# Optimization experiments

Hardware: AMD Instinct MI355X
Metric: run time of the kernel (lower is better)

The kernel has to match this reference:

```python
import jax, jax.numpy as jnp
import numpy as np

VOCAB = 50000
EMB = 200        # embedding_size
CAP = 3          # capitalization_size
IN = EMB + CAP   # LSTM input size = 203
HID = 128        # LSTMCell(128)
B = 256
T = 500          # comment_length
NC = 6           # num_classes
DENSE = 64


def _lstm_scan(x_tbi, W, b):
    """x_tbi: [T,B,IN]. W: [IN+HID, 4*HID] (tf gate order i, j, f, o), b: [4*HID].
    Returns h sequence [T,B,HID]. forget_bias=1.0 as in tf.contrib.rnn.LSTMCell."""
    h0 = jnp.zeros((x_tbi.shape[1], HID), x_tbi.dtype)

    def step(carry, x):
        h, c = carry
        gates = jnp.concatenate([x, h], axis=-1) @ W + b   # [B, 4*HID]
        i, j, f, o = jnp.split(gates, 4, axis=-1)
        c = jax.nn.sigmoid(f + 1.0) * c + jax.nn.sigmoid(i) * jnp.tanh(j)
        h = jax.nn.sigmoid(o) * jnp.tanh(c)
        return (h, c), h

    _, hs = jax.lax.scan(step, (h0, h0), x_tbi)
    return hs


def setup_inputs() -> dict:
    key = jax.random.key(0)
    ks = jax.random.split(key, 12)
    words = jax.random.randint(ks[0], (B, T), 0, VOCAB, dtype=jnp.int32)
    capitals = jax.random.randint(ks[1], (B, T), 0, CAP, dtype=jnp.int32)
    # word embeddings: random trainable table with a trailing zero-padding row
    word_emb = jax.random.normal(ks[2], (VOCAB + 1, EMB), dtype=jnp.float32) * 0.1
    # capitalization embedding: one_hot_embedding_matrix(3) = [eye(3); zeros(1,3)]
    cap_emb = jnp.concatenate([jnp.eye(CAP, dtype=jnp.float32),
                               jnp.zeros((1, CAP), dtype=jnp.float32)], axis=0)
    def glorot(k, shape):
        lim = np.sqrt(6.0 / (shape[0] + shape[1]))
        return jax.random.uniform(k, shape, jnp.float32, -lim, lim)
    W_fw = glorot(ks[3], (IN + HID, 4 * HID))
    b_fw = jnp.zeros((4 * HID,), jnp.float32)
    W_bw = glorot(ks[4], (IN + HID, 4 * HID))
    b_bw = jnp.zeros((4 * HID,), jnp.float32)
    W1 = glorot(ks[5], (2 * HID, DENSE))
    b1 = jnp.zeros((DENSE,), jnp.float32)
    W2 = glorot(ks[6], (DENSE, NC))
    b2 = jnp.zeros((NC,), jnp.float32)
    return {"words": words, "capitals": capitals, "word_emb": word_emb,
            "cap_emb": cap_emb, "W_fw": W_fw, "b_fw": b_fw,
            "W_bw": W_bw, "b_bw": b_bw, "W1": W1, "b1": b1,
            "W2": W2, "b2": b2}


def reference(words, capitals, word_emb, cap_emb, W_fw, b_fw, W_bw, b_bw,
              W1, b1, W2, b2):
    # embedding lookups and concat -> [B, T, 203]
    x = jnp.concatenate([word_emb[words], cap_emb[capitals]], axis=-1)
    x_tbi = jnp.transpose(x, (1, 0, 2))                    # [T, B, IN]
    # forward direction: take output at last timestep
    h_fw_last = _lstm_scan(x_tbi, W_fw, b_fw)[-1]          # [B, HID]
    # backward direction: bidirectional_dynamic_rnn reverses bw outputs back,
    # so outputs[1][:, 0, :] == last state of scan over the reversed sequence
    h_bw_first = _lstm_scan(x_tbi[::-1], W_bw, b_bw)[-1]   # [B, HID]
    rnn_output = jnp.concatenate([h_fw_last, h_bw_first], axis=1)  # [B, 256]
    dense1 = jax.nn.elu(rnn_output @ W1 + b1)              # [B, 64]
    y_hat = jax.nn.sigmoid(dense1 @ W2 + b2)               # [B, NC]
    return y_hat
```

## Files before the change

kernel.cpp:

```cpp
#include <hip/hip_runtime.h>

#define T 500
#define NB 256
#define VROWS 50001
#define EMB 200
#define KPAD 224
#define MPAD 50048

typedef unsigned short u16;
typedef __attribute__((ext_vector_type(8))) __bf16 bf16x8;
typedef __attribute__((ext_vector_type(8))) short short8;
typedef __attribute__((ext_vector_type(4))) float f32x4;
typedef __attribute__((ext_vector_type(4))) u16 u16x4;
typedef __attribute__((ext_vector_type(4))) int i32x4;

__device__ __forceinline__ u16 f2bf(float x) {
  __bf16 h = (__bf16)x;
  return __builtin_bit_cast(u16, h);
}
__device__ __forceinline__ float bf2f(u16 b) {
  union { unsigned u; float f; } v; v.u = ((unsigned)b) << 16;
  return v.f;
}
__device__ __forceinline__ float rcp_(float x) { return __builtin_amdgcn_rcpf(x); }
__device__ __forceinline__ float sig_(float x) { return rcp_(1.f + __expf(-x)); }
__device__ __forceinline__ float tanh_(float x) { return 1.f - 2.f * rcp_(1.f + __expf(2.f * x)); }

__global__ void prep_kernel(const int* __restrict__ words, const int* __restrict__ caps,
                            const float* __restrict__ word_emb,
                            const float* __restrict__ cap_emb,
                            const float* __restrict__ Wfw, const float* __restrict__ bfw,
                            const float* __restrict__ Wbw, const float* __restrict__ bbw,
                            int* __restrict__ wordsT, int* __restrict__ capsT,
                            float* __restrict__ Cproj, u16* __restrict__ Apad,
                            u16* __restrict__ Bt) {
  const int S0 = NB * T;
  const int S1 = MPAD * (KPAD / 4);
  const int S2 = 2 * 512 * KPAD;
  const int S3 = 2 * 4 * 512;
  int tid = blockIdx.x * blockDim.x + threadIdx.x;
  int nthr = gridDim.x * blockDim.x;
  for (int i = tid; i < S0 + S1 + S2 + S3; i += nthr) {
    if (i < S0) {
      int b = i / T, t = i - b * T;
      wordsT[t * NB + b] = words[i];
      capsT[t * NB + b]  = caps[i];
    } else if (i < S0 + S1) {
      int idx = i - S0;
      int v = idx / (KPAD / 4), q = idx - v * (KPAD / 4);
      int k = q * 4;
      u16x4 o;
      if (v < VROWS && k < EMB) {
        const float* p = word_emb + (size_t)v * EMB + k;
        o[0] = f2bf(p[0]); o[1] = f2bf(p[1]); o[2] = f2bf(p[2]); o[3] = f2bf(p[3]);
      } else {
        o[0] = o[1] = o[2] = o[3] = 0;
      }
      *(u16x4*)(Apad + (size_t)v * KPAD + k) = o;
    } else if (i < S0 + S1 + S2) {
      int idx = i - S0 - S1;
      int d = idx / (512 * KPAD), rem = idx - d * (512 * KPAD);
      int colp = rem / KPAD, k = rem - colp * KPAD;
      const float* W = d ? Wbw : Wfw;
      int g = colp & 3, jj = colp >> 2;
      Bt[idx] = (k < EMB) ? f2bf(W[k * 512 + g * 128 + jj]) : (u16)0;
    } else {
      int idx = i - S0 - S1 - S2;
      int dir = idx >> 11; int c = (idx >> 9) & 3; int colp = idx & 511;
      int j = colp >> 2, g = colp & 3;
      const float* W = dir ? Wbw : Wfw;
      const float* bias = dir ? bbw : bfw;
      float v = bias[g * 128 + j];
      #pragma unroll
      for (int cc = 0; cc < 3; ++cc)
        v += cap_emb[c * 3 + cc] * W[(200 + cc) * 512 + g * 128 + j];
      Cproj[idx] = v;
    }
  }
}

__global__ __launch_bounds__(256) void vproj_kernel(
    const u16* __restrict__ Apad, const u16* __restrict__ Bt,
    u16* __restrict__ Vfw, u16* __restrict__ Vbw) {
  const int mt = blockIdx.x, nt = blockIdx.y, dir = blockIdx.z;
  const u16* __restrict__ B = Bt + (size_t)dir * 512 * KPAD;
  u16* __restrict__ V = dir ? Vbw : Vfw;

  __shared__ u16 Al[2][128 * 32];
  __shared__ u16 Bl[2][128 * 32];

  const int tid = threadIdx.x;
  const int w = tid >> 6, l = tid & 63;
  const int la = l & 15, lb = l >> 4;
  const int m0 = mt * 128, n0 = nt * 128;

  auto stage = [&](int buf, int ks) {
    int k0 = ks * 32;
    #pragma unroll
    for (int h = 0; h < 2; ++h) {
      int c = w * 128 + h * 64 + l;
      int row = c >> 2, kq = c & 3;
      const u16* ga = Apad + (size_t)(m0 + row) * KPAD + k0 + kq * 8;
      __builtin_amdgcn_global_load_lds(
          (const __attribute__((address_space(1))) void*)ga,
          (__attribute__((address_space(3))) void*)&Al[buf][(w * 128 + h * 64) * 8],
          16, 0, 0);
      const u16* gb = B + (size_t)(n0 + row) * KPAD + k0 + kq * 8;
      __builtin_amdgcn_global_load_lds(
          (const __attribute__((address_space(1))) void*)gb,
          (__attribute__((address_space(3))) void*)&Bl[buf][(w * 128 + h * 64) * 8],
          16, 0, 0);
    }
  };

  f32x4 z = {0.f, 0.f, 0.f, 0.f};
  f32x4 acc[4][4] = {{z,z,z,z},{z,z,z,z},{z,z,z,z},{z,z,z,z}};
  const int wr = w >> 1, wc = w & 1;

  stage(0, 0);
  __syncthreads();
  #pragma unroll 1
  for (int ks = 0; ks < 7; ++ks) {
    int cur = ks & 1;
    if (ks < 6) stage(cur ^ 1, ks + 1);
    bf16x8 af[4], bfr[4];
    #pragma unroll
    for (int m = 0; m < 4; ++m)
      af[m] = *(const bf16x8*)&Al[cur][(wr * 64 + m * 16 + la) * 32 + lb * 8];
    #pragma unroll
    for (int n = 0; n < 4; ++n)
      bfr[n] = *(const bf16x8*)&Bl[cur][(wc * 64 + n * 16 + la) * 32 + lb * 8];
    #pragma unroll
    for (int m = 0; m < 4; ++m)
      #pragma unroll
      for (int n = 0; n < 4; ++n)
        acc[m][n] = __builtin_amdgcn_mfma_f32_16x16x32_bf16(af[m], bfr[n], acc[m][n], 0, 0, 0);
    __syncthreads();
  }

  #pragma unroll
  for (int m = 0; m < 4; ++m) {
    #pragma unroll
    for (int n = 0; n < 4; ++n) {
      #pragma unroll
      for (int r = 0; r < 4; ++r) {
        int v = m0 + wr * 64 + m * 16 + lb * 4 + r;
        int colp = n0 + wc * 64 + n * 16 + la;
        V[(size_t)v * 512 + colp] = f2bf(acc[m][n][r]);
      }
    }
  }
}

template <int PAR>
__device__ __forceinline__ void lstm_step(
    int t, int dir, int b0, int la, int lb, int j,
    const int* __restrict__ wordsT, const int* __restrict__ capsT,
    const u16* __restrict__ V, const float* __restrict__ Cp,
    const bf16x8 (&bfrag)[4][4], u16* __restrict__ hbuf,
    u16x4 (&vw_c)[4], f32x4 (&cp_c)[4],
    i32x4& wi_c, i32x4& ci_c,
    i32x4& wi_g, i32x4& ci_g,
    u16x4 (&vw_g)[4], f32x4 (&cp_g)[4],
    f32x4& cst, f32x4& hl) {
  {
    int ts = t + 4; if (ts > T - 1) ts = T - 1;
    int tt = dir ? (T - 1 - ts) : ts;
    wi_c = *(const i32x4*)(wordsT + tt * NB + b0 + lb * 4);
    ci_c = *(const i32x4*)(capsT + tt * NB + b0 + lb * 4);
  }
  #pragma unroll
  for (int r = 0; r < 4; ++r) {
    vw_g[r] = *(const u16x4*)(V + (size_t)wi_g[r] * 512 + j * 4);
    cp_g[r] = *(const f32x4*)(Cp + ci_g[r] * 512 + j * 4);
  }

  const u16* hb = hbuf + PAR * 2048;
  const int swz = (la & 7) << 3;
  bf16x8 afr[4];
  #pragma unroll
  for (int kk = 0; kk < 4; ++kk)
    afr[kk] = *(const bf16x8*)(hb + ((la * 128 + kk * 32 + lb * 8) ^ swz));

  f32x4 acc0, acc1, acc2, acc3;
  #pragma unroll
  for (int r = 0; r < 4; ++r) {
    acc0[r] = bf2f(vw_c[r][0]) + cp_c[r][0];
    acc1[r] = bf2f(vw_c[r][1]) + cp_c[r][1];
    acc2[r] = bf2f(vw_c[r][2]) + cp_c[r][2];
    acc3[r] = bf2f(vw_c[r][3]) + cp_c[r][3];
  }
  #pragma unroll
  for (int kk = 0; kk < 4; ++kk) {
    acc0 = __builtin_amdgcn_mfma_f32_16x16x32_bf16(afr[kk], bfrag[0][kk], acc0, 0, 0, 0);
    acc1 = __builtin_amdgcn_mfma_f32_16x16x32_bf16(afr[kk], bfrag[1][kk], acc1, 0, 0, 0);
    acc2 = __builtin_amdgcn_mfma_f32_16x16x32_bf16(afr[kk], bfrag[2][kk], acc2, 0, 0, 0);
    acc3 = __builtin_amdgcn_mfma_f32_16x16x32_bf16(afr[kk], bfrag[3][kk], acc3, 0, 0, 0);
  }
  u16* ho = hbuf + (PAR ^ 1) * 2048;
  #pragma unroll
  for (int r = 0; r < 4; ++r) {
    float fg = sig_(acc2[r] + 1.f);
    float ig = sig_(acc0[r]);
    float tj = tanh_(acc1[r]);
    float cn = fg * cst[r] + ig * tj;
    cst[r] = cn;
    float hn = sig_(acc3[r]) * tanh_(cn);
    hl[r] = hn;
    int row = lb * 4 + r;
    ho[(row * 128 + j) ^ ((row & 7) << 3)] = f2bf(hn);
  }
  asm volatile("s_waitcnt lgkmcnt(0)\n\ts_barrier" ::: "memory");
}

__global__ __launch_bounds__(512, 1) void lstm_kernel(
    const int* __restrict__ wordsT, const int* __restrict__ capsT,
    const u16* __restrict__ Vfw, const u16* __restrict__ Vbw,
    const float* __restrict__ CprojAll, const float* __restrict__ Wfw,
    const float* __restrict__ Wbw, float* __restrict__ rnn) {
  const int dir = blockIdx.x & 1;
  const int chunk = blockIdx.x >> 1;
  const int b0 = chunk * 16;
  const u16* __restrict__ V = dir ? Vbw : Vfw;
  const float* __restrict__ Cp = CprojAll + dir * 4 * 512;
  const float* __restrict__ W = dir ? Wbw : Wfw;

  const int tid = threadIdx.x;
  const int w = tid >> 6, l = tid & 63, la = l & 15, lb = l >> 4;
  const int j = w * 16 + la;

  bf16x8 bfrag[4][4];
  #pragma unroll
  for (int g = 0; g < 4; ++g) {
    #pragma unroll
    for (int kk = 0; kk < 4; ++kk) {
      short8 t8;
      #pragma unroll
      for (int r = 0; r < 8; ++r) {
        int k = kk * 32 + lb * 8 + r;
        t8[r] = (short)f2bf(W[(203 + k) * 512 + g * 128 + j]);
      }
      bfrag[g][kk] = __builtin_bit_cast(bf16x8, t8);
    }
  }

  __shared__ u16 hbuf[2 * 16 * 128];
  for (int i = tid; i < 2 * 16 * 128; i += 512) hbuf[i] = 0;

  f32x4 cst = {0.f, 0.f, 0.f, 0.f};
  f32x4 hl  = {0.f, 0.f, 0.f, 0.f};

  i32x4 wiA, ciA, wiB, ciB, wiC, ciC, wiD, ciD;
  u16x4 vwA[4], vwB[4], vwC[4], vwD[4];
  f32x4 cpA[4], cpB[4], cpC[4], cpD[4];
  {
    int t0 = dir ? (T - 1) : 0;
    int t1 = dir ? (T - 2) : 1;
    int t2 = dir ? (T - 3) : 2;
    int t3 = dir ? (T - 4) : 3;
    wiA = *(const i32x4*)(wordsT + t0 * NB + b0 + lb * 4);
    ciA = *(const i32x4*)(capsT + t0 * NB + b0 + lb * 4);
    wiB = *(const i32x4*)(wordsT + t1 * NB + b0 + lb * 4);
    ciB = *(const i32x4*)(capsT + t1 * NB + b0 + lb * 4);
    wiC = *(const i32x4*)(wordsT + t2 * NB + b0 + lb * 4);
    ciC = *(const i32x4*)(capsT + t2 * NB + b0 + lb * 4);
    wiD = *(const i32x4*)(wordsT + t3 * NB + b0 + lb * 4);
    ciD = *(const i32x4*)(capsT + t3 * NB + b0 + lb * 4);
  }
  #pragma unroll
  for (int r = 0; r < 4; ++r) {
    vwA[r] = *(const u16x4*)(V + (size_t)wiA[r] * 512 + j * 4);
    cpA[r] = *(const f32x4*)(Cp + ciA[r] * 512 + j * 4);
    vwB[r] = *(const u16x4*)(V + (size_t)wiB[r] * 512 + j * 4);
    cpB[r] = *(const f32x4*)(Cp + ciB[r] * 512 + j * 4);
  }
  __syncthreads();

  #pragma unroll 1
  for (int tq = 0; tq < T / 4; ++tq) {
    int t0 = 4 * tq;
    lstm_step<0>(t0,     dir, b0, la, lb, j, wordsT, capsT, V, Cp, bfrag, hbuf,
                 vwA, cpA, wiA, ciA, wiC, ciC, vwC, cpC, cst, hl);
    lstm_step<1>(t0 + 1, dir, b0, la, lb, j, wordsT, capsT, V, Cp, bfrag, hbuf,
                 vwB, cpB, wiB, ciB, wiD, ciD, vwD, cpD, cst, hl);
    lstm_step<0>(t0 + 2, dir, b0, la, lb, j, wordsT, capsT, V, Cp, bfrag, hbuf,
                 vwC, cpC, wiC, ciC, wiA, ciA, vwA, cpA, cst, hl);
    lstm_step<1>(t0 + 3, dir, b0, la, lb, j, wordsT, capsT, V, Cp, bfrag, hbuf,
                 vwD, cpD, wiD, ciD, wiB, ciB, vwB, cpB, cst, hl);
  }

  #pragma unroll
  for (int r = 0; r < 4; ++r)
    rnn[(size_t)(b0 + lb * 4 + r) * 256 + dir * 128 + j] = hl[r];
}

__global__ void head_kernel(const float* __restrict__ rnn, const float* __restrict__ W1,
                            const float* __restrict__ b1, const float* __restrict__ W2,
                            const float* __restrict__ b2, float* __restrict__ out) {
  int b = blockIdx.x;
  int jj = threadIdx.x;
  __shared__ float d1[64];
  float acc = b1[jj];
  const float* r = rnn + b * 256;
  #pragma unroll 4
  for (int k = 0; k < 256; ++k) acc += r[k] * W1[k * 64 + jj];
  d1[jj] = acc > 0.f ? acc : (__expf(acc) - 1.f);
  __syncthreads();
  if (jj < 6) {
    float a2 = b2[jj];
    #pragma unroll 8
    for (int k = 0; k < 64; ++k) a2 += d1[k] * W2[k * 6 + jj];
    out[b * 6 + jj] = rcp_(1.f + __expf(-a2));
  }
}

extern "C" void kernel_launch(void* const* d_in, const int* in_sizes, int n_in,
                              void* d_out, int out_size, void* d_ws, size_t ws_size,
                              hipStream_t stream) {
  (void)in_sizes; (void)n_in; (void)out_size; (void)ws_size;
  const int*   words    = (const int*)  d_in[0];
  const int*   caps     = (const int*)  d_in[1];
  const float* word_emb = (const float*)d_in[2];
  const float* cap_emb  = (const float*)d_in[3];
  const float* Wfw      = (const float*)d_in[4];
  const float* bfw      = (const float*)d_in[5];
  const float* Wbw      = (const float*)d_in[6];
  const float* bbw      = (const float*)d_in[7];
  const float* W1       = (const float*)d_in[8];
  const float* b1       = (const float*)d_in[9];
  const float* W2       = (const float*)d_in[10];
  const float* b2       = (const float*)d_in[11];
  float* out = (float*)d_out;

  char* base = (char*)d_ws;
  size_t off = 0;
  auto alloc = [&](size_t bytes) {
    char* q = base + off;
    off = (off + bytes + 255) & ~(size_t)255;
    return q;
  };
  u16*   Vfw    = (u16*)  alloc((size_t)MPAD * 512 * 2);
  u16*   Vbw    = (u16*)  alloc((size_t)MPAD * 512 * 2);
  u16*   Apad   = (u16*)  alloc((size_t)MPAD * KPAD * 2);
  u16*   Bt     = (u16*)  alloc((size_t)2 * 512 * KPAD * 2);
  int*   wordsT = (int*)  alloc((size_t)T * NB * 4);
  int*   capsT  = (int*)  alloc((size_t)T * NB * 4);
  float* Cproj  = (float*)alloc((size_t)2 * 4 * 512 * 4);
  float* rnn    = (float*)alloc((size_t)256 * 256 * 4);

  hipLaunchKernelGGL(prep_kernel, dim3(2048), dim3(256), 0, stream,
                     words, caps, word_emb, cap_emb, Wfw, bfw, Wbw, bbw,
                     wordsT, capsT, Cproj, Apad, Bt);
  hipLaunchKernelGGL(vproj_kernel, dim3(MPAD / 128, 4, 2), dim3(256), 0, stream,
                     Apad, Bt, Vfw, Vbw);
  hipLaunchKernelGGL(lstm_kernel, dim3(32), dim3(512), 0, stream,
                     wordsT, capsT, Vfw, Vbw, Cproj, Wfw, Wbw, rnn);
  hipLaunchKernelGGL(head_kernel, dim3(256), dim3(64), 0, stream,
                     rnn, W1, b1, W2, b2, out);
}
```

Before: 633.0 us.

## Split LSTM batch across four times more blocks and prescale gates for exp2

The recurrent LSTM kernel now gives each workgroup 4 batch rows instead of 16, launching 128 workgroups instead of 32 so more compute units share the serial time loop. Only the first row-group of lanes gathers the embedding projections. After the MFMAs, shuffles hand each lane a single gate element, so every lane evaluates one cell instead of four, which shortens the per-step nonlinearity tail. The gate scale factors (negative log2e, doubled for the tanh gate) and the forget bias are folded into the weights and Cproj at prep time, so the activations use raw exp2. The cost is that three quarters of each 16-row MFMA tile now does wasted work on zero rows, and bf16 rounding is applied to the scaled weights.

```diff
diff --git a/kernel.cpp b/kernel.cpp
--- a/kernel.cpp
+++ b/kernel.cpp
@@ -6,6 +6,7 @@
 #define EMB 200
 #define KPAD 224
 #define MPAD 50048
+#define LOG2E 1.44269504f
 
 typedef unsigned short u16;
 typedef __attribute__((ext_vector_type(8))) __bf16 bf16x8;
@@ -23,8 +24,8 @@
   return v.f;
 }
 __device__ __forceinline__ float rcp_(float x) { return __builtin_amdgcn_rcpf(x); }
-__device__ __forceinline__ float sig_(float x) { return rcp_(1.f + __expf(-x)); }
-__device__ __forceinline__ float tanh_(float x) { return 1.f - 2.f * rcp_(1.f + __expf(2.f * x)); }
+__device__ __forceinline__ float ex2_(float x) { return __builtin_amdgcn_exp2f(x); }
+__device__ __forceinline__ float gsc(int g) { return (g == 1) ? 2.f * LOG2E : -LOG2E; }
 
 __global__ void prep_kernel(const int* __restrict__ words, const int* __restrict__ caps,
                             const float* __restrict__ word_emb,
@@ -63,18 +64,18 @@
       int colp = rem / KPAD, k = rem - colp * KPAD;
       const float* W = d ? Wbw : Wfw;
       int g = colp & 3, jj = colp >> 2;
-      Bt[idx] = (k < EMB) ? f2bf(W[k * 512 + g * 128 + jj]) : (u16)0;
+      Bt[idx] = (k < EMB) ? f2bf(W[k * 512 + g * 128 + jj] * gsc(g)) : (u16)0;
     } else {
       int idx = i - S0 - S1 - S2;
       int dir = idx >> 11; int c = (idx >> 9) & 3; int colp = idx & 511;
       int j = colp >> 2, g = colp & 3;
       const float* W = dir ? Wbw : Wfw;
       const float* bias = dir ? bbw : bfw;
-      float v = bias[g * 128 + j];
+      float v = bias[g * 128 + j] + (g == 2 ? 1.f : 0.f);
       #pragma unroll
       for (int cc = 0; cc < 3; ++cc)
         v += cap_emb[c * 3 + cc] * W[(200 + cc) * 512 + g * 128 + j];
-      Cproj[idx] = v;
+      Cproj[idx] = v * gsc(g);
     }
   }
 }
@@ -162,17 +163,19 @@
     i32x4& wi_c, i32x4& ci_c,
     i32x4& wi_g, i32x4& ci_g,
     u16x4 (&vw_g)[4], f32x4 (&cp_g)[4],
-    f32x4& cst, f32x4& hl) {
+    float& cst, float& hl) {
   {
     int ts = t + 4; if (ts > T - 1) ts = T - 1;
     int tt = dir ? (T - 1 - ts) : ts;
-    wi_c = *(const i32x4*)(wordsT + tt * NB + b0 + lb * 4);
-    ci_c = *(const i32x4*)(capsT + tt * NB + b0 + lb * 4);
-  }
-  #pragma unroll
-  for (int r = 0; r < 4; ++r) {
-    vw_g[r] = *(const u16x4*)(V + (size_t)wi_g[r] * 512 + j * 4);
-    cp_g[r] = *(const f32x4*)(Cp + ci_g[r] * 512 + j * 4);
+    wi_c = *(const i32x4*)(wordsT + tt * NB + b0);
+    ci_c = *(const i32x4*)(capsT + tt * NB + b0);
+  }
+  if (lb == 0) {
+    #pragma unroll
+    for (int r = 0; r < 4; ++r) {
+      vw_g[r] = *(const u16x4*)(V + (size_t)wi_g[r] * 512 + j * 4);
+      cp_g[r] = *(const f32x4*)(Cp + ci_g[r] * 512 + j * 4);
+    }
   }
 
   const u16* hb = hbuf + PAR * 2048;
@@ -197,19 +200,29 @@
     acc2 = __builtin_amdgcn_mfma_f32_16x16x32_bf16(afr[kk], bfrag[2][kk], acc2, 0, 0, 0);
     acc3 = __builtin_amdgcn_mfma_f32_16x16x32_bf16(afr[kk], bfrag[3][kk], acc3, 0, 0, 0);
   }
+
+  float a0, a1, a2, a3;
+  #pragma unroll
+  for (int r = 0; r < 4; ++r) {
+    float t0 = __shfl(acc0[r], la, 64);
+    float t1 = __shfl(acc1[r], la, 64);
+    float t2 = __shfl(acc2[r], la, 64);
+    float t3 = __shfl(acc3[r], la, 64);
+    if (lb == r) { a0 = t0; a1 = t1; a2 = t2; a3 = t3; }
+  }
+
+  float ig = rcp_(1.f + ex2_(a0));
+  float tj = 1.f - 2.f * rcp_(1.f + ex2_(a1));
+  float fg = rcp_(1.f + ex2_(a2));
+  float cn = fg * cst + ig * tj;
+  cst = cn;
+  float og = rcp_(1.f + ex2_(a3));
+  float hn = og * (1.f - 2.f * rcp_(1.f + ex2_(2.f * LOG2E * cn)));
+  hl = hn;
+
   u16* ho = hbuf + (PAR ^ 1) * 2048;
-  #pragma unroll
-  for (int r = 0; r < 4; ++r) {
-    float fg = sig_(acc2[r] + 1.f);
-    float ig = sig_(acc0[r]);
-    float tj = tanh_(acc1[r]);
-    float cn = fg * cst[r] + ig * tj;
-    cst[r] = cn;
-    float hn = sig_(acc3[r]) * tanh_(cn);
-    hl[r] = hn;
-    int row = lb * 4 + r;
-    ho[(row * 128 + j) ^ ((row & 7) << 3)] = f2bf(hn);
-  }
+  ho[(lb * 128 + j) ^ ((lb & 7) << 3)] = f2bf(hn);
+
   asm volatile("s_waitcnt lgkmcnt(0)\n\ts_barrier" ::: "memory");
 }
 
@@ -220,7 +233,7 @@
     const float* __restrict__ Wbw, float* __restrict__ rnn) {
   const int dir = blockIdx.x & 1;
   const int chunk = blockIdx.x >> 1;
-  const int b0 = chunk * 16;
+  const int b0 = chunk * 4;
   const u16* __restrict__ V = dir ? Vbw : Vfw;
   const float* __restrict__ Cp = CprojAll + dir * 4 * 512;
   const float* __restrict__ W = dir ? Wbw : Wfw;
@@ -238,7 +251,7 @@
       #pragma unroll
       for (int r = 0; r < 8; ++r) {
         int k = kk * 32 + lb * 8 + r;
-        t8[r] = (short)f2bf(W[(203 + k) * 512 + g * 128 + j]);
+        t8[r] = (short)f2bf(W[(203 + k) * 512 + g * 128 + j] * gsc(g));
       }
       bfrag[g][kk] = __builtin_bit_cast(bf16x8, t8);
     }
@@ -247,32 +260,40 @@
   __shared__ u16 hbuf[2 * 16 * 128];
   for (int i = tid; i < 2 * 16 * 128; i += 512) hbuf[i] = 0;
 
-  f32x4 cst = {0.f, 0.f, 0.f, 0.f};
-  f32x4 hl  = {0.f, 0.f, 0.f, 0.f};
+  float cst = 0.f, hl = 0.f;
 
   i32x4 wiA, ciA, wiB, ciB, wiC, ciC, wiD, ciD;
   u16x4 vwA[4], vwB[4], vwC[4], vwD[4];
   f32x4 cpA[4], cpB[4], cpC[4], cpD[4];
+  #pragma unroll
+  for (int r = 0; r < 4; ++r) {
+    vwA[r] = u16x4{0,0,0,0}; vwB[r] = u16x4{0,0,0,0};
+    vwC[r] = u16x4{0,0,0,0}; vwD[r] = u16x4{0,0,0,0};
+    cpA[r] = f32x4{0,0,0,0}; cpB[r] = f32x4{0,0,0,0};
+    cpC[r] = f32x4{0,0,0,0}; cpD[r] = f32x4{0,0,0,0};
+  }
   {
     int t0 = dir ? (T - 1) : 0;
     int t1 = dir ? (T - 2) : 1;
     int t2 = dir ? (T - 3) : 2;
     int t3 = dir ? (T - 4) : 3;
-    wiA = *(const i32x4*)(wordsT + t0 * NB + b0 + lb * 4);
-    ciA = *(const i32x4*)(capsT + t0 * NB + b0 + lb * 4);
-    wiB = *(const i32x4*)(wordsT + t1 * NB + b0 + lb * 4);
-    ciB = *(const i32x4*)(capsT + t1 * NB + b0 + lb * 4);
-    wiC = *(const i32x4*)(wordsT + t2 * NB + b0 + lb * 4);
-    ciC = *(const i32x4*)(capsT + t2 * NB + b0 + lb * 4);
-    wiD = *(const i32x4*)(wordsT + t3 * NB + b0 + lb * 4);
-    ciD = *(const i32x4*)(capsT + t3 * NB + b0 + lb * 4);
-  }
-  #pragma unroll
-  for (int r = 0; r < 4; ++r) {
-    vwA[r] = *(const u16x4*)(V + (size_t)wiA[r] * 512 + j * 4);
-    cpA[r] = *(const f32x4*)(Cp + ciA[r] * 512 + j * 4);
-    vwB[r] = *(const u16x4*)(V + (size_t)wiB[r] * 512 + j * 4);
-    cpB[r] = *(const f32x4*)(Cp + ciB[r] * 512 + j * 4);
+    wiA = *(const i32x4*)(wordsT + t0 * NB + b0);
+    ciA = *(const i32x4*)(capsT + t0 * NB + b0);
+    wiB = *(const i32x4*)(wordsT + t1 * NB + b0);
+    ciB = *(const i32x4*)(capsT + t1 * NB + b0);
+    wiC = *(const i32x4*)(wordsT + t2 * NB + b0);
+    ciC = *(const i32x4*)(capsT + t2 * NB + b0);
+    wiD = *(const i32x4*)(wordsT + t3 * NB + b0);
+    ciD = *(const i32x4*)(capsT + t3 * NB + b0);
+  }
+  if (lb == 0) {
+    #pragma unroll
+    for (int r = 0; r < 4; ++r) {
+      vwA[r] = *(const u16x4*)(V + (size_t)wiA[r] * 512 + j * 4);
+      cpA[r] = *(const f32x4*)(Cp + ciA[r] * 512 + j * 4);
+      vwB[r] = *(const u16x4*)(V + (size_t)wiB[r] * 512 + j * 4);
+      cpB[r] = *(const f32x4*)(Cp + ciB[r] * 512 + j * 4);
+    }
   }
   __syncthreads();
 
@@ -289,9 +310,7 @@
                  vwD, cpD, wiD, ciD, wiB, ciB, vwB, cpB, cst, hl);
   }
 
-  #pragma unroll
-  for (int r = 0; r < 4; ++r)
-    rnn[(size_t)(b0 + lb * 4 + r) * 256 + dir * 128 + j] = hl[r];
+  rnn[(size_t)(b0 + lb) * 256 + dir * 128 + j] = hl;
 }
 
 __global__ void head_kernel(const float* __restrict__ rnn, const float* __restrict__ W1,
@@ -353,7 +372,7 @@
                      wordsT, capsT, Cproj, Apad, Bt);
   hipLaunchKernelGGL(vproj_kernel, dim3(MPAD / 128, 4, 2), dim3(256), 0, stream,
                      Apad, Bt, Vfw, Vbw);
-  hipLaunchKernelGGL(lstm_kernel, dim3(32), dim3(512), 0, stream,
+  hipLaunchKernelGGL(lstm_kernel, dim3(128), dim3(512), 0, stream,
                      wordsT, capsT, Vfw, Vbw, Cproj, Wfw, Wbw, rnn);
   hipLaunchKernelGGL(head_kernel, dim3(256), dim3(64), 0, stream,
                      rnn, W1, b1, W2, b2, out);
```

Result: slower. 730.2 us (+15.4%).
